# Performance work log

Hardware: AMD Instinct MI355X
Metric: run time of the kernel (lower is better)

## Reference

```python
import jax, jax.numpy as jnp
import numpy as np


def segment_softmax(x, seg, num_segments):
    # numerically-stable softmax over graph segments (rows of the sparse matrix)
    m = jax.ops.segment_max(x, seg, num_segments=num_segments)
    e = jnp.exp(x - m[seg])
    s = jax.ops.segment_sum(e, seg, num_segments=num_segments)
    return e / s[seg]


def setup_inputs() -> dict:
    key = jax.random.key(0)
    ks = jax.random.split(key, 12)
    B, N, E, P, H = 256, 51200, 102400, 5, 300
    instruction = jax.random.normal(ks[0], (B, H), dtype=jnp.float32)
    distribution = jax.random.uniform(ks[1], (N,), dtype=jnp.float32)
    node_attrs = jax.random.normal(ks[2], (N, H), dtype=jnp.float32)
    edge_attrs = jax.random.normal(ks[3], (E, H), dtype=jnp.float32)
    node_indices = jnp.sort(jax.random.randint(ks[4], (N,), 0, B)).astype(jnp.int32)
    edge_batch_indices = jax.random.randint(ks[5], (E,), 0, B).astype(jnp.int32)
    edge_indices = jax.random.randint(ks[6], (2, E), 0, N).astype(jnp.int32)
    prop_embeds = jax.random.normal(ks[7], (P, H), dtype=jnp.float32)
    Ws_property = jax.random.uniform(ks[8], (P, H, H), dtype=jnp.float32)
    W_state = jax.random.uniform(ks[9], (H,), dtype=jnp.float32)
    W_relation = jax.random.uniform(ks[10], (H,), dtype=jnp.float32)
    return {"instruction": instruction, "distribution": distribution, "node_attrs": node_attrs,
            "edge_attrs": edge_attrs, "node_indices": node_indices,
            "edge_batch_indices": edge_batch_indices, "edge_indices": edge_indices,
            "prop_embeds": prop_embeds, "Ws_property": Ws_property,
            "W_state": W_state, "W_relation": W_relation}


def reference(instruction, distribution, node_attrs, edge_attrs, node_indices,
              edge_batch_indices, edge_indices, prop_embeds, Ws_property,
              W_state, W_relation):
    B = instruction.shape[0]
    # [B, P] property similarities
    prop_sim = jax.nn.softmax(instruction @ prop_embeds.T, axis=1)
    ps_node = prop_sim[node_indices]            # [N, P]
    instr_node = instruction[node_indices]      # [N, H]
    # per-property transform of node attrs: [N, P-1, H]
    wx = jnp.einsum('phk,nk->nph', Ws_property[:-1], node_attrs)
    node_scores = jax.nn.elu(jnp.sum(ps_node[:, :-1, None] * instr_node[:, None, :] * wx, axis=1))  # [N, H]
    # relation transform of edge attrs: [E, H]
    edge_wx = jnp.einsum('hk,ek->eh', Ws_property[-1], edge_attrs)
    edge_scores = jax.nn.elu(instruction[edge_batch_indices] * edge_wx)  # [E, H]
    # per-graph (segment) softmax over state logits
    state_logits = node_scores @ W_state        # [N]
    next_states = segment_softmax(state_logits, node_indices, B)
    # scatter-add message passing: dst node accumulates distribution[src] * edge_scores
    agg = jnp.zeros_like(node_scores).at[edge_indices[1]].add(
        distribution[edge_indices[0], None] * edge_scores)  # [N, H]
    rel_logits = agg @ W_relation               # [N]
    next_relations = segment_softmax(rel_logits, node_indices, B)
    r = ps_node[:, -1]
    next_distribution = r * next_relations + (1.0 - r) * next_states
    return next_distribution, prop_sim
```

## Files before the change

kernel.cpp:

```cpp
#include <hip/hip_runtime.h>
#include <math.h>

#define H 300
#define PP 5
#define NE 64
#define KC 32
#define NCH 10
#define WROWS 320
#define ROWB 128
#define WTILE (WROWS * ROWB)
#define ATILE (NE * ROWB)
#define NTHREADS 256

using short8 = __attribute__((ext_vector_type(8))) short;
using f32x4  = __attribute__((ext_vector_type(4))) float;

__device__ __forceinline__ float wsum64(float v) {
#pragma unroll
    for (int m = 32; m >= 1; m >>= 1) v += __shfl_xor(v, m, 64);
    return v;
}
__device__ __forceinline__ float wmax64(float v) {
#pragma unroll
    for (int m = 32; m >= 1; m >>= 1) v = fmaxf(v, __shfl_xor(v, m, 64));
    return v;
}
__device__ __forceinline__ float eluf(float x) { return x > 0.f ? x : expm1f(x); }

__device__ __forceinline__ unsigned short f2bf(float x) {
    unsigned int u = __float_as_uint(x);
    unsigned int r = u + 0x7FFF + ((u >> 16) & 1);
    return (unsigned short)(r >> 16);
}
__device__ __forceinline__ float bf2f(unsigned short h) {
    return __uint_as_float(((unsigned int)h) << 16);
}
__device__ __forceinline__ int sw(int r, int kb) {
    return r * ROWB + (kb ^ ((r & 7) << 4));
}
__device__ __forceinline__ void split4(const float* v, uint2& ph, uint2& pl) {
    unsigned short hs[4], ls[4];
#pragma unroll
    for (int i = 0; i < 4; ++i) {
        hs[i] = f2bf(v[i]);
        ls[i] = f2bf(v[i] - bf2f(hs[i]));
    }
    ph = make_uint2((unsigned)hs[0] | ((unsigned)hs[1] << 16),
                    (unsigned)hs[2] | ((unsigned)hs[3] << 16));
    pl = make_uint2((unsigned)ls[0] | ((unsigned)ls[1] << 16),
                    (unsigned)ls[2] | ((unsigned)ls[3] << 16));
}
__device__ __forceinline__ void gload16(const void* g, void* lds) {
    __builtin_amdgcn_global_load_lds(
        (const __attribute__((address_space(1))) unsigned int*)g,
        (__attribute__((address_space(3))) unsigned int*)lds, 16, 0, 0);
}

__global__ void k_prop_sim(const float* __restrict__ instr,
                           const float* __restrict__ pe,
                           float* __restrict__ prop_sim) {
    int b = blockIdx.x, lane = threadIdx.x;
    float dots[PP];
#pragma unroll
    for (int p = 0; p < PP; ++p) {
        float s = 0.f;
        for (int hh = lane; hh < H; hh += 64) s += instr[b * H + hh] * pe[p * H + hh];
        dots[p] = wsum64(s);
    }
    if (lane == 0) {
        float m = dots[0];
#pragma unroll
        for (int p = 1; p < PP; ++p) m = fmaxf(m, dots[p]);
        float e[PP], s = 0.f;
#pragma unroll
        for (int p = 0; p < PP; ++p) { e[p] = expf(dots[p] - m); s += e[p]; }
        float inv = 1.f / s;
#pragma unroll
        for (int p = 0; p < PP; ++p) prop_sim[b * PP + p] = e[p] * inv;
    }
}

__global__ void k_counts(const int* __restrict__ idx, int* __restrict__ counts, int N) {
    int i = blockIdx.x * blockDim.x + threadIdx.x;
    if (i < N) atomicAdd(&counts[idx[i]], 1);
}

__global__ void k_scan(const int* __restrict__ counts, int* __restrict__ offsets, int B) {
    __shared__ int sh[256];
    int t = threadIdx.x;
    int c = (t < B) ? counts[t] : 0;
    sh[t] = c;
    __syncthreads();
    for (int off = 1; off < 256; off <<= 1) {
        int v = (t >= off) ? sh[t - off] : 0;
        __syncthreads();
        sh[t] += v;
        __syncthreads();
    }
    if (t < B) offsets[t] = sh[t] - c;
    if (t == B - 1) offsets[B] = sh[t];
}

__global__ void k_presplit(const float* __restrict__ W4, char* __restrict__ img) {
    int c = blockIdx.x;
    int idx = blockIdx.y * NTHREADS + threadIdx.x;
    int r = idx >> 3, j = idx & 7;
    int k = c * KC + j * 4;
    float v[4] = {0.f, 0.f, 0.f, 0.f};
    if (r < H && k < H) *(float4*)v = *(const float4*)&W4[(size_t)r * H + k];
    uint2 ph, pl;
    split4(v, ph, pl);
    char* row = img + (size_t)c * WTILE + (size_t)r * ROWB;
    int x = (r & 7) << 4;
    *(uint2*)(row + ((j * 8) ^ x)) = ph;
    *(uint2*)(row + ((64 + j * 8) ^ x)) = pl;
}

__global__ void k_combine(const float* __restrict__ Ws,
                          const float* __restrict__ prop_sim,
                          char* __restrict__ img) {
    int b = blockIdx.x, c = blockIdx.y, t = threadIdx.x;
    float ps0 = prop_sim[b * PP + 0], ps1 = prop_sim[b * PP + 1];
    float ps2 = prop_sim[b * PP + 2], ps3 = prop_sim[b * PP + 3];
    char* tile = img + ((size_t)b * NCH + c) * WTILE;
#pragma unroll
    for (int i = 0; i < 10; ++i) {
        int idx = t + i * NTHREADS;
        int r = idx >> 3, j = idx & 7;
        int k = c * KC + j * 4;
        float cv[4] = {0.f, 0.f, 0.f, 0.f};
        if (r < H && k < H) {
            size_t base = (size_t)r * H + k;
            float w0[4], w1[4], w2[4], w3[4];
            *(float4*)w0 = *(const float4*)&Ws[0 * (size_t)H * H + base];
            *(float4*)w1 = *(const float4*)&Ws[1 * (size_t)H * H + base];
            *(float4*)w2 = *(const float4*)&Ws[2 * (size_t)H * H + base];
            *(float4*)w3 = *(const float4*)&Ws[3 * (size_t)H * H + base];
#pragma unroll
            for (int q = 0; q < 4; ++q)
                cv[q] = fmaf(ps0, w0[q], fmaf(ps1, w1[q], fmaf(ps2, w2[q], ps3 * w3[q])));
        }
        uint2 ph, pl;
        split4(cv, ph, pl);
        char* row = tile + (size_t)r * ROWB;
        int x = (r & 7) << 4;
        *(uint2*)(row + ((j * 8) ^ x)) = ph;
        *(uint2*)(row + ((64 + j * 8) ^ x)) = pl;
    }
}

__global__ __launch_bounds__(NTHREADS, 3) void k_node(
    const float* __restrict__ na, const char* __restrict__ Wimg,
    const float* __restrict__ instr, const float* __restrict__ wstate,
    const int* __restrict__ offsets, float* __restrict__ slog, int N)
{
    __shared__ __align__(16) char W_t[WTILE];
    __shared__ __align__(16) char A_t[ATILE];

    int b = blockIdx.y;
    int start = offsets[b], end = offsets[b + 1];
    int n0 = start + blockIdx.x * NE;
    if (n0 >= end) return;
    int nn = min(NE, end - n0);

    int t = threadIdx.x;
    int w = t >> 6, l = t & 63, lane16 = l & 15, g = l >> 4;
    int wn = w & 1, wh = w >> 1;
    const char* Wsrc = Wimg + (size_t)b * NCH * WTILE;

    f32x4 acc[10][2];
#pragma unroll
    for (int ht = 0; ht < 10; ++ht)
#pragma unroll
        for (int cg = 0; cg < 2; ++cg) acc[ht][cg] = (f32x4){0.f, 0.f, 0.f, 0.f};

    float4 pa[2];
    auto loadA = [&](int c) {
#pragma unroll
        for (int i = 0; i < 2; ++i) {
            int idx = t + i * NTHREADS;
            int r = idx >> 3, j = idx & 7;
            int k = c * KC + j * 4;
            float4 v = {0.f, 0.f, 0.f, 0.f};
            if (k < H) {
                int row = min(n0 + r, N - 1);
                v = *(const float4*)&na[(size_t)row * H + k];
            }
            pa[i] = v;
        }
    };
    auto storeA = [&]() {
#pragma unroll
        for (int i = 0; i < 2; ++i) {
            int idx = t + i * NTHREADS;
            int r = idx >> 3, j = idx & 7;
            float v[4] = {pa[i].x, pa[i].y, pa[i].z, pa[i].w};
            uint2 ph, pl;
            split4(v, ph, pl);
            *(uint2*)(A_t + sw(r, j * 8)) = ph;
            *(uint2*)(A_t + sw(r, 64 + j * 8)) = pl;
        }
    };
    auto gloadW = [&](int c) {
        const char* src = Wsrc + (size_t)c * WTILE;
        int off0 = (t >> 6) * 1024 + (t & 63) * 16;
        int loff0 = (t >> 6) * 1024;
#pragma unroll
        for (int s = 0; s < 10; ++s)
            gload16(src + s * 4096 + off0, W_t + s * 4096 + loff0);
    };

    loadA(0);
    storeA();
    gloadW(0);
    loadA(1);
    __syncthreads();

    for (int c = 0; c < NCH; ++c) {
        short8 bh[2], bl[2];
#pragma unroll
        for (int cg = 0; cg < 2; ++cg) {
            int brow = wn * 32 + cg * 16 + lane16;
            bh[cg] = *(const short8*)(A_t + sw(brow, g * 16));
            bl[cg] = *(const short8*)(A_t + sw(brow, 64 + g * 16));
        }
#pragma unroll
        for (int ht = 0; ht < 10; ++ht) {
            int arow = (wh * 10 + ht) * 16 + lane16;
            short8 ah = *(const short8*)(W_t + sw(arow, g * 16));
            short8 al = *(const short8*)(W_t + sw(arow, 64 + g * 16));
#pragma unroll
            for (int cg = 0; cg < 2; ++cg) {
                acc[ht][cg] = __builtin_amdgcn_mfma_f32_16x16x32_bf16(ah, bh[cg], acc[ht][cg], 0, 0, 0);
                acc[ht][cg] = __builtin_amdgcn_mfma_f32_16x16x32_bf16(ah, bl[cg], acc[ht][cg], 0, 0, 0);
                acc[ht][cg] = __builtin_amdgcn_mfma_f32_16x16x32_bf16(al, bh[cg], acc[ht][cg], 0, 0, 0);
            }
        }
        if (c + 1 < NCH) {
            __syncthreads();
            storeA();
            gloadW(c + 1);
            if (c + 2 < NCH) loadA(c + 2);
            __syncthreads();
        }
    }

    const float* insb = instr + (size_t)b * H;
#pragma unroll
    for (int cg = 0; cg < 2; ++cg) {
        float part = 0.f;
#pragma unroll
        for (int ht = 0; ht < 10; ++ht) {
            int hb = wh * 160 + ht * 16 + g * 4;
#pragma unroll
            for (int r = 0; r < 4; ++r) {
                int h = hb + r;
                if (h < H) part += wstate[h] * eluf(insb[h] * acc[ht][cg][r]);
            }
        }
        part += __shfl_xor(part, 16, 64);
        part += __shfl_xor(part, 32, 64);
        int col = wn * 32 + cg * 16 + lane16;
        if (l < 16 && col < nn) atomicAdd(&slog[n0 + col], part);
    }
}

__global__ __launch_bounds__(NTHREADS, 3) void k_edge(
    const float* __restrict__ ea, const char* __restrict__ Wimg,
    const float* __restrict__ instr, const float* __restrict__ wrel,
    const int* __restrict__ eb, const int* __restrict__ ei,
    const float* __restrict__ dist, float* __restrict__ rlog, int E)
{
    __shared__ __align__(16) char W_t[WTILE];
    __shared__ __align__(16) char A_t[ATILE];

    int e0 = blockIdx.x * NE;
    int t = threadIdx.x;
    int w = t >> 6, l = t & 63, lane16 = l & 15, g = l >> 4;
    int wn = w & 1, wh = w >> 1;

    f32x4 acc[10][2];
#pragma unroll
    for (int ht = 0; ht < 10; ++ht)
#pragma unroll
        for (int cg = 0; cg < 2; ++cg) acc[ht][cg] = (f32x4){0.f, 0.f, 0.f, 0.f};

    float4 pa[2];
    auto loadA = [&](int c) {
#pragma unroll
        for (int i = 0; i < 2; ++i) {
            int idx = t + i * NTHREADS;
            int r = idx >> 3, j = idx & 7;
            int k = c * KC + j * 4;
            float4 v = {0.f, 0.f, 0.f, 0.f};
            if (k < H) v = *(const float4*)&ea[(size_t)(e0 + r) * H + k];
            pa[i] = v;
        }
    };
    auto storeA = [&]() {
#pragma unroll
        for (int i = 0; i < 2; ++i) {
            int idx = t + i * NTHREADS;
            int r = idx >> 3, j = idx & 7;
            float v[4] = {pa[i].x, pa[i].y, pa[i].z, pa[i].w};
            uint2 ph, pl;
            split4(v, ph, pl);
            *(uint2*)(A_t + sw(r, j * 8)) = ph;
            *(uint2*)(A_t + sw(r, 64 + j * 8)) = pl;
        }
    };
    auto gloadW = [&](int c) {
        const char* src = Wimg + (size_t)c * WTILE;
        int off0 = (t >> 6) * 1024 + (t & 63) * 16;
        int loff0 = (t >> 6) * 1024;
#pragma unroll
        for (int s = 0; s < 10; ++s)
            gload16(src + s * 4096 + off0, W_t + s * 4096 + loff0);
    };

    loadA(0);
    storeA();
    gloadW(0);
    loadA(1);
    __syncthreads();

    for (int c = 0; c < NCH; ++c) {
        short8 bh[2], bl[2];
#pragma unroll
        for (int cg = 0; cg < 2; ++cg) {
            int brow = wn * 32 + cg * 16 + lane16;
            bh[cg] = *(const short8*)(A_t + sw(brow, g * 16));
            bl[cg] = *(const short8*)(A_t + sw(brow, 64 + g * 16));
        }
#pragma unroll
        for (int ht = 0; ht < 10; ++ht) {
            int arow = (wh * 10 + ht) * 16 + lane16;
            short8 ah = *(const short8*)(W_t + sw(arow, g * 16));
            short8 al = *(const short8*)(W_t + sw(arow, 64 + g * 16));
#pragma unroll
            for (int cg = 0; cg < 2; ++cg) {
                acc[ht][cg] = __builtin_amdgcn_mfma_f32_16x16x32_bf16(ah, bh[cg], acc[ht][cg], 0, 0, 0);
                acc[ht][cg] = __builtin_amdgcn_mfma_f32_16x16x32_bf16(ah, bl[cg], acc[ht][cg], 0, 0, 0);
                acc[ht][cg] = __builtin_amdgcn_mfma_f32_16x16x32_bf16(al, bh[cg], acc[ht][cg], 0, 0, 0);
            }
        }
        if (c + 1 < NCH) {
            __syncthreads();
            storeA();
            gloadW(c + 1);
            if (c + 2 < NCH) loadA(c + 2);
            __syncthreads();
        }
    }

#pragma unroll
    for (int cg = 0; cg < 2; ++cg) {
        int e = e0 + wn * 32 + cg * 16 + lane16;
        int be = eb[e];
        const float* insb = instr + (size_t)be * H;
        float part = 0.f;
#pragma unroll
        for (int ht = 0; ht < 10; ++ht) {
            int hb = wh * 160 + ht * 16 + g * 4;
#pragma unroll
            for (int r = 0; r < 4; ++r) {
                int h = hb + r;
                if (h < H) part += wrel[h] * eluf(insb[h] * acc[ht][cg][r]);
            }
        }
        part += __shfl_xor(part, 16, 64);
        part += __shfl_xor(part, 32, 64);
        if (l < 16) atomicAdd(&rlog[ei[E + e]], dist[ei[e]] * part);
    }
}

__global__ void k_final(const float* __restrict__ slog, const float* __restrict__ rlog,
                        const float* __restrict__ prop_sim, const int* __restrict__ offsets,
                        float* __restrict__ out)
{
    int b = blockIdx.x;
    int s0 = offsets[b], e1 = offsets[b + 1];
    int t = threadIdx.x, wave = t >> 6, lane = t & 63;
    __shared__ float shA[4], shB[4];
    float mS = -3.0e38f, mR = -3.0e38f;
    for (int i = s0 + t; i < e1; i += 256) {
        mS = fmaxf(mS, slog[i]);
        mR = fmaxf(mR, rlog[i]);
    }
    mS = wmax64(mS); mR = wmax64(mR);
    if (lane == 0) { shA[wave] = mS; shB[wave] = mR; }
    __syncthreads();
    mS = fmaxf(fmaxf(shA[0], shA[1]), fmaxf(shA[2], shA[3]));
    mR = fmaxf(fmaxf(shB[0], shB[1]), fmaxf(shB[2], shB[3]));
    __syncthreads();
    float sS = 0.f, sR = 0.f;
    for (int i = s0 + t; i < e1; i += 256) {
        sS += expf(slog[i] - mS);
        sR += expf(rlog[i] - mR);
    }
    sS = wsum64(sS); sR = wsum64(sR);
    if (lane == 0) { shA[wave] = sS; shB[wave] = sR; }
    __syncthreads();
    sS = shA[0] + shA[1] + shA[2] + shA[3];
    sR = shB[0] + shB[1] + shB[2] + shB[3];
    float r = prop_sim[b * PP + (PP - 1)];
    float iS = 1.f / sS, iR = 1.f / sR;
    for (int i = s0 + t; i < e1; i += 256) {
        float ns = expf(slog[i] - mS) * iS;
        float nr = expf(rlog[i] - mR) * iR;
        out[i] = r * nr + (1.f - r) * ns;
    }
}

extern "C" void kernel_launch(void* const* d_in, const int* in_sizes, int n_in,
                              void* d_out, int out_size, void* d_ws, size_t ws_size,
                              hipStream_t stream) {
    (void)n_in; (void)out_size; (void)ws_size;
    const float* instruction  = (const float*)d_in[0];
    const float* distribution = (const float*)d_in[1];
    const float* node_attrs   = (const float*)d_in[2];
    const float* edge_attrs   = (const float*)d_in[3];
    const int*   node_indices = (const int*)d_in[4];
    const int*   edge_batch   = (const int*)d_in[5];
    const int*   edge_indices = (const int*)d_in[6];
    const float* prop_embeds  = (const float*)d_in[7];
    const float* Ws           = (const float*)d_in[8];
    const float* W_state      = (const float*)d_in[9];
    const float* W_rel        = (const float*)d_in[10];

    int B = in_sizes[0] / H;
    int N = in_sizes[1];
    int E = in_sizes[5];

    float* out = (float*)d_out;
    float* prop_sim = out + N;

    float* ws = (float*)d_ws;
    float* state_logits = ws;
    float* rel_logits   = ws + N;
    int*   offsets      = (int*)(ws + 2 * (size_t)N);
    int*   counts       = offsets + (B + 1);
    uintptr_t wsp = (uintptr_t)(counts + B);
    wsp = (wsp + 255) & ~(uintptr_t)255;
    char* Wr_img = (char*)wsp;
    char* Wc_img = Wr_img + (size_t)NCH * WTILE;

    size_t zero_bytes = (size_t)2 * N * sizeof(float) + (size_t)(2 * B + 1) * sizeof(int);
    hipMemsetAsync(d_ws, 0, zero_bytes, stream);

    k_prop_sim<<<B, 64, 0, stream>>>(instruction, prop_embeds, prop_sim);
    k_presplit<<<dim3(NCH, 10), NTHREADS, 0, stream>>>(Ws + 4 * (size_t)H * H, Wr_img);
    k_counts<<<(N + 255) / 256, 256, 0, stream>>>(node_indices, counts, N);
    k_scan<<<1, 256, 0, stream>>>(counts, offsets, B);
    k_combine<<<dim3(B, NCH), NTHREADS, 0, stream>>>(Ws, prop_sim, Wc_img);
    k_node<<<dim3(6, B), NTHREADS, 0, stream>>>(node_attrs, Wc_img, instruction,
                                                W_state, offsets, state_logits, N);
    k_edge<<<E / NE, NTHREADS, 0, stream>>>(edge_attrs, Wr_img, instruction, W_rel,
                                            edge_batch, edge_indices,
                                            distribution, rel_logits, E);
    k_final<<<B, 256, 0, stream>>>(state_logits, rel_logits, prop_sim, offsets, out);
}
```

Measured before the change: 366.1 us.

## Double block tile to 128 rows with 512 threads and hand-tuned barriers

```diff
diff --git a/kernel.cpp b/kernel.cpp
--- a/kernel.cpp
+++ b/kernel.cpp
@@ -3,7 +3,7 @@
 
 #define H 300
 #define PP 5
-#define NE 64
+#define NE 128
 #define KC 32
 #define NCH 10
 #define WROWS 320
@@ -11,6 +11,7 @@
 #define WTILE (WROWS * ROWB)
 #define ATILE (NE * ROWB)
 #define NTHREADS 256
+#define GT 512
 
 using short8 = __attribute__((ext_vector_type(8))) short;
 using f32x4  = __attribute__((ext_vector_type(4))) float;
@@ -55,6 +56,11 @@
         (const __attribute__((address_space(1))) unsigned int*)g,
         (__attribute__((address_space(3))) unsigned int*)lds, 16, 0, 0);
 }
+#define SBAR() __builtin_amdgcn_s_barrier()
+#define SCHED() __builtin_amdgcn_sched_barrier(0)
+#define WAIT_LGKM() asm volatile("s_waitcnt lgkmcnt(0)" ::: "memory")
+#define WAIT_VM2()  asm volatile("s_waitcnt vmcnt(2) lgkmcnt(0)" ::: "memory")
+#define WAIT_VM0()  asm volatile("s_waitcnt vmcnt(0) lgkmcnt(0)" ::: "memory")
 
 __global__ void k_prop_sim(const float* __restrict__ instr,
                            const float* __restrict__ pe,
@@ -149,7 +155,7 @@
     }
 }
 
-__global__ __launch_bounds__(NTHREADS, 3) void k_node(
+__global__ __launch_bounds__(GT, 4) void k_node(
     const float* __restrict__ na, const char* __restrict__ Wimg,
     const float* __restrict__ instr, const float* __restrict__ wstate,
     const int* __restrict__ offsets, float* __restrict__ slog, int N)
@@ -165,7 +171,7 @@
 
     int t = threadIdx.x;
     int w = t >> 6, l = t & 63, lane16 = l & 15, g = l >> 4;
-    int wn = w & 1, wh = w >> 1;
+    int wn = w & 3, wh = w >> 2;
     const char* Wsrc = Wimg + (size_t)b * NCH * WTILE;
 
     f32x4 acc[10][2];
@@ -178,7 +184,7 @@
     auto loadA = [&](int c) {
 #pragma unroll
         for (int i = 0; i < 2; ++i) {
-            int idx = t + i * NTHREADS;
+            int idx = t + i * GT;
             int r = idx >> 3, j = idx & 7;
             int k = c * KC + j * 4;
             float4 v = {0.f, 0.f, 0.f, 0.f};
@@ -192,7 +198,7 @@
     auto storeA = [&]() {
 #pragma unroll
         for (int i = 0; i < 2; ++i) {
-            int idx = t + i * NTHREADS;
+            int idx = t + i * GT;
             int r = idx >> 3, j = idx & 7;
             float v[4] = {pa[i].x, pa[i].y, pa[i].z, pa[i].w};
             uint2 ph, pl;
@@ -203,18 +209,22 @@
     };
     auto gloadW = [&](int c) {
         const char* src = Wsrc + (size_t)c * WTILE;
-        int off0 = (t >> 6) * 1024 + (t & 63) * 16;
-        int loff0 = (t >> 6) * 1024;
-#pragma unroll
-        for (int s = 0; s < 10; ++s)
-            gload16(src + s * 4096 + off0, W_t + s * 4096 + loff0);
+        int goff = w * 5120 + (t & 63) * 16;
+        int loff = w * 5120;
+#pragma unroll
+        for (int s = 0; s < 5; ++s)
+            gload16(src + s * 1024 + goff, W_t + s * 1024 + loff);
     };
 
     loadA(0);
     storeA();
     gloadW(0);
+    SCHED();
     loadA(1);
-    __syncthreads();
+    SCHED();
+    WAIT_VM2();
+    SBAR();
+    SCHED();
 
     for (int c = 0; c < NCH; ++c) {
         short8 bh[2], bl[2];
@@ -237,11 +247,21 @@
             }
         }
         if (c + 1 < NCH) {
-            __syncthreads();
+            WAIT_LGKM();
+            SBAR();
+            SCHED();
             storeA();
             gloadW(c + 1);
-            if (c + 2 < NCH) loadA(c + 2);
-            __syncthreads();
+            SCHED();
+            if (c + 2 < NCH) {
+                loadA(c + 2);
+                SCHED();
+                WAIT_VM2();
+            } else {
+                WAIT_VM0();
+            }
+            SBAR();
+            SCHED();
         }
     }
 
@@ -265,7 +285,7 @@
     }
 }
 
-__global__ __launch_bounds__(NTHREADS, 3) void k_edge(
+__global__ __launch_bounds__(GT, 4) void k_edge(
     const float* __restrict__ ea, const char* __restrict__ Wimg,
     const float* __restrict__ instr, const float* __restrict__ wrel,
     const int* __restrict__ eb, const int* __restrict__ ei,
@@ -277,7 +297,7 @@
     int e0 = blockIdx.x * NE;
     int t = threadIdx.x;
     int w = t >> 6, l = t & 63, lane16 = l & 15, g = l >> 4;
-    int wn = w & 1, wh = w >> 1;
+    int wn = w & 3, wh = w >> 2;
 
     f32x4 acc[10][2];
 #pragma unroll
@@ -289,7 +309,7 @@
     auto loadA = [&](int c) {
 #pragma unroll
         for (int i = 0; i < 2; ++i) {
-            int idx = t + i * NTHREADS;
+            int idx = t + i * GT;
             int r = idx >> 3, j = idx & 7;
             int k = c * KC + j * 4;
             float4 v = {0.f, 0.f, 0.f, 0.f};
@@ -300,7 +320,7 @@
     auto storeA = [&]() {
 #pragma unroll
         for (int i = 0; i < 2; ++i) {
-            int idx = t + i * NTHREADS;
+            int idx = t + i * GT;
             int r = idx >> 3, j = idx & 7;
             float v[4] = {pa[i].x, pa[i].y, pa[i].z, pa[i].w};
             uint2 ph, pl;
@@ -311,18 +331,22 @@
     };
     auto gloadW = [&](int c) {
         const char* src = Wimg + (size_t)c * WTILE;
-        int off0 = (t >> 6) * 1024 + (t & 63) * 16;
-        int loff0 = (t >> 6) * 1024;
-#pragma unroll
-        for (int s = 0; s < 10; ++s)
-            gload16(src + s * 4096 + off0, W_t + s * 4096 + loff0);
+        int goff = w * 5120 + (t & 63) * 16;
+        int loff = w * 5120;
+#pragma unroll
+        for (int s = 0; s < 5; ++s)
+            gload16(src + s * 1024 + goff, W_t + s * 1024 + loff);
     };
 
     loadA(0);
     storeA();
     gloadW(0);
+    SCHED();
     loadA(1);
-    __syncthreads();
+    SCHED();
+    WAIT_VM2();
+    SBAR();
+    SCHED();
 
     for (int c = 0; c < NCH; ++c) {
         short8 bh[2], bl[2];
@@ -345,11 +369,21 @@
             }
         }
         if (c + 1 < NCH) {
-            __syncthreads();
+            WAIT_LGKM();
+            SBAR();
+            SCHED();
             storeA();
             gloadW(c + 1);
-            if (c + 2 < NCH) loadA(c + 2);
-            __syncthreads();
+            SCHED();
+            if (c + 2 < NCH) {
+                loadA(c + 2);
+                SCHED();
+                WAIT_VM2();
+            } else {
+                WAIT_VM0();
+            }
+            SBAR();
+            SCHED();
         }
     }
 
@@ -453,10 +487,10 @@
     k_counts<<<(N + 255) / 256, 256, 0, stream>>>(node_indices, counts, N);
     k_scan<<<1, 256, 0, stream>>>(counts, offsets, B);
     k_combine<<<dim3(B, NCH), NTHREADS, 0, stream>>>(Ws, prop_sim, Wc_img);
-    k_node<<<dim3(6, B), NTHREADS, 0, stream>>>(node_attrs, Wc_img, instruction,
-                                                W_state, offsets, state_logits, N);
-    k_edge<<<E / NE, NTHREADS, 0, stream>>>(edge_attrs, Wr_img, instruction, W_rel,
-                                            edge_batch, edge_indices,
-                                            distribution, rel_logits, E);
+    k_node<<<dim3(3, B), GT, 0, stream>>>(node_attrs, Wc_img, instruction,
+                                          W_state, offsets, state_logits, N);
+    k_edge<<<E / NE, GT, 0, stream>>>(edge_attrs, Wr_img, instruction, W_rel,
+                                      edge_batch, edge_indices,
+                                      distribution, rel_logits, E);
     k_final<<<B, 256, 0, stream>>>(state_logits, rel_logits, prop_sim, offsets, out);
 }
```

After: 482.6 us. 1.32x slower.
